# Optimization experiments

Measured on AMD Instinct MI355X. Metric: run time of the kernel, lower is better.

Reference implementation:

```python
import jax, jax.numpy as jnp
import numpy as np

N_NEURONS = 100000
N_EDGES = 5000000
N_TYPES = 64
N_DM = 512
BATCH = 16
LAYER_NUMBER = 4  # number of connectome hops


def setup_inputs() -> dict:
    key = jax.random.key(0)
    ks = jax.random.split(key, 11)
    return {
        "x": jax.random.normal(ks[0], (N_NEURONS, BATCH), dtype=jnp.float32),
        "type_weight": jax.random.normal(ks[1], (N_TYPES,), dtype=jnp.float32),
        "type_bias": jax.random.normal(ks[2], (N_TYPES,), dtype=jnp.float32),
        # shared_weights = log1p(synapse counts) -> positive; use uniform
        "edge_weights": jax.random.uniform(ks[3], (N_EDGES,), dtype=jnp.float32),
        "dm_vals": jax.random.uniform(ks[4], (N_DM,), dtype=jnp.float32),
        "fc_w": jax.random.normal(ks[5], (1, N_DM), dtype=jnp.float32) * 0.04,
        "fc_b": jax.random.normal(ks[6], (1,), dtype=jnp.float32),
        "cell_type_indices": jax.random.randint(ks[7], (N_NEURONS,), 0, N_TYPES),
        "edge_rows": jax.random.randint(ks[8], (N_EDGES,), 0, N_NEURONS),
        "edge_cols": jax.random.randint(ks[9], (N_EDGES,), 0, N_NEURONS),
        "dm_cols": jax.random.randint(ks[10], (N_DM,), 0, N_NEURONS),
    }


def reference(x, type_weight, type_bias, edge_weights, dm_vals, fc_w, fc_b,
              cell_type_indices, edge_rows, edge_cols, dm_cols):
    # RetinaConnectionLayer: per-cell-type 1->1 linear (gathered scale + bias)
    h = x * type_weight[cell_type_indices][:, None] + type_bias[cell_type_indices][:, None]
    # AdultConnectome / SparseMatrixMul: repeated sparse COO matmul h = A @ h
    # with shared per-edge weights, applied layer_number times.
    for _ in range(LAYER_NUMBER):
        contrib = edge_weights[:, None] * h[edge_cols]          # [E, B] gather
        h = jax.ops.segment_sum(contrib, edge_rows, num_segments=N_NEURONS)
    # torch.sparse.mm(decision_making_tensor, h): row-selection sparse matrix
    y = dm_vals[:, None] * h[dm_cols]                           # [N_DM, B]
    # final_fc over the decision-neuron axis
    out = y.T @ fc_w.T + fc_b                                   # [B, 1]
    return out
```

## Files before the change

kernel.cpp:

```cpp
#include <hip/hip_runtime.h>

#define NN 100000
#define NE 5000000
#define NB 16
#define NDM 512

#define RPB 1024
#define NBUCKET 98
#define CAP 55296
#define CHUNK 8192
#define NCHUNK ((NE + CHUNK - 1) / CHUNK)
#define SUB 16
#define NWAVE 16

__global__ void setup(const float* __restrict__ dmv, const int* __restrict__ dmc,
                      const float* __restrict__ fcw,
                      float* __restrict__ u0, int* __restrict__ cursor) {
    int t = threadIdx.x;
    if (t < NDM) atomicAdd(&u0[dmc[t]], dmv[t] * fcw[t]);
    if (t < NBUCKET) cursor[t] = t * CAP;
}

__global__ void scatter_fused(const int* __restrict__ er, const int* __restrict__ ec,
                              const float* __restrict__ ew,
                              const float* __restrict__ u0, float* __restrict__ u1,
                              int* __restrict__ cursor, int2* __restrict__ packed) {
    __shared__ int hist[NWAVE][NBUCKET];
    __shared__ __align__(16) int sdst[CHUNK];
    int tid = threadIdx.x;
    int wv = tid >> 6;
    for (int k = tid; k < NWAVE * NBUCKET; k += 1024) hist[k / NBUCKET][k % NBUCKET] = 0;
    __syncthreads();
    int base = blockIdx.x * CHUNK;
    int n = min(CHUNK, NE - base);
    const int4* ec4 = (const int4*)(ec + base);
    for (int k = tid; k < (n >> 2); k += 1024) {
        int4 c = ec4[k];
        ((int4*)sdst)[k] = c;
        atomicAdd(&hist[wv][c.x >> 10], 1);
        atomicAdd(&hist[wv][c.y >> 10], 1);
        atomicAdd(&hist[wv][c.z >> 10], 1);
        atomicAdd(&hist[wv][c.w >> 10], 1);
    }
    __syncthreads();
    for (int b = tid; b < NBUCKET; b += 1024) {
        int pre[NWAVE];
        int c = 0;
        #pragma unroll
        for (int w = 0; w < NWAVE; ++w) { pre[w] = c; c += hist[w][b]; }
        int gb = c ? atomicAdd(&cursor[b], c) : 0;
        #pragma unroll
        for (int w = 0; w < NWAVE; ++w) hist[w][b] = gb + pre[w];
    }
    __syncthreads();
    const int4*   er4 = (const int4*)(er + base);
    const float4* ew4 = (const float4*)(ew + base);
    for (int k = tid; k < (n >> 2); k += 1024) {
        int4 r = er4[k];
        float4 w = ew4[k];
        int k4 = 4 * k;
        int d, pos;
        float a;
        d = sdst[k4];     pos = atomicAdd(&hist[wv][d >> 10], 1);
        packed[pos] = make_int2(((d & 1023) << 17) | r.x, __float_as_int(w.x));
        a = u0[r.x]; if (a != 0.f) atomicAdd(&u1[d], w.x * a);
        d = sdst[k4 + 1]; pos = atomicAdd(&hist[wv][d >> 10], 1);
        packed[pos] = make_int2(((d & 1023) << 17) | r.y, __float_as_int(w.y));
        a = u0[r.y]; if (a != 0.f) atomicAdd(&u1[d], w.y * a);
        d = sdst[k4 + 2]; pos = atomicAdd(&hist[wv][d >> 10], 1);
        packed[pos] = make_int2(((d & 1023) << 17) | r.z, __float_as_int(w.z));
        a = u0[r.z]; if (a != 0.f) atomicAdd(&u1[d], w.z * a);
        d = sdst[k4 + 3]; pos = atomicAdd(&hist[wv][d >> 10], 1);
        packed[pos] = make_int2(((d & 1023) << 17) | r.w, __float_as_int(w.w));
        a = u0[r.w]; if (a != 0.f) atomicAdd(&u1[d], w.w * a);
    }
}

__global__ void spmv_sorted(const int* __restrict__ cursor,
                            const int2* __restrict__ packed,
                            const float* __restrict__ wc, float* __restrict__ wn) {
    __shared__ float acc[RPB];
    int bucket = blockIdx.x >> 4;
    int sub = blockIdx.x & (SUB - 1);
    int t = threadIdx.x;
    #pragma unroll
    for (int k = 0; k < 4; ++k) acc[t + 256 * k] = 0.f;
    __syncthreads();
    int s = bucket * CAP;
    int e = cursor[bucket];
    int cnt = e - s;
    int slice = (cnt + SUB - 1) >> 4;
    int mys = s + sub * slice;
    int mye = min(mys + slice, e);
    int i = mys + t;
    for (; i + 256 < mye; i += 512) {
        int2 p0 = packed[i];
        int2 p1 = packed[i + 256];
        float v0 = __int_as_float(p0.y) * wc[p0.x & 0x1FFFF];
        float v1 = __int_as_float(p1.y) * wc[p1.x & 0x1FFFF];
        if (v0 != 0.f) atomicAdd(&acc[p0.x >> 17], v0);
        if (v1 != 0.f) atomicAdd(&acc[p1.x >> 17], v1);
    }
    if (i < mye) {
        int2 p = packed[i];
        float v = __int_as_float(p.y) * wc[p.x & 0x1FFFF];
        if (v != 0.f) atomicAdd(&acc[p.x >> 17], v);
    }
    __syncthreads();
    #pragma unroll
    for (int k = 0; k < 4; ++k) {
        int row = bucket * RPB + t + 256 * k;
        float a = acc[t + 256 * k];
        if (a != 0.f && row < NN) atomicAdd(&wn[row], a);
    }
}

__global__ void final_dot(const float* __restrict__ x, const float* __restrict__ tw,
                          const float* __restrict__ tb, const int* __restrict__ ct,
                          const float* __restrict__ u,
                          float* __restrict__ acc_out) {
    __shared__ float s[512];
    __shared__ float sred[256][4];
    __shared__ float sbias[4];
    int tid = threadIdx.x;
    int base = blockIdx.x * 512;
    int nrows = min(512, NN - base);
    float accb = 0.f;
    for (int r = tid; r < nrows; r += 256) {
        int n = base + r;
        float un = u[n];
        int t = ct[n];
        s[r] = un * tw[t];
        accb = fmaf(un, tb[t], accb);
    }
    __syncthreads();
    float a0 = 0.f, a1 = 0.f, a2 = 0.f, a3 = 0.f;
    int j = (tid & 3) * 4;
    for (int r = tid >> 2; r < nrows; r += 64) {
        float4 xv = *(const float4*)&x[(size_t)(base + r) * NB + j];
        float sv = s[r];
        a0 = fmaf(sv, xv.x, a0);
        a1 = fmaf(sv, xv.y, a1);
        a2 = fmaf(sv, xv.z, a2);
        a3 = fmaf(sv, xv.w, a3);
    }
    sred[tid][0] = a0; sred[tid][1] = a1; sred[tid][2] = a2; sred[tid][3] = a3;
    for (int off = 32; off; off >>= 1) accb += __shfl_down(accb, off);
    if ((tid & 63) == 0) sbias[tid >> 6] = accb;
    __syncthreads();
    if (tid < 16) {
        int q = tid >> 2, k = tid & 3;
        float sum = 0.f;
        for (int i = 0; i < 64; ++i) sum += sred[q + 4 * i][k];
        atomicAdd(&acc_out[tid], sum);
    }
    if (tid == 16)
        atomicAdd(&acc_out[16], sbias[0] + sbias[1] + sbias[2] + sbias[3]);
}

__global__ void finalize(const float* __restrict__ acc, const float* __restrict__ fcb,
                         float* __restrict__ out) {
    int b = threadIdx.x;
    if (b < NB) out[b] = acc[b] + acc[16] + fcb[0];
}

extern "C" void kernel_launch(void* const* d_in, const int* in_sizes, int n_in,
                              void* d_out, int out_size, void* d_ws, size_t ws_size,
                              hipStream_t stream) {
    const float* x   = (const float*)d_in[0];
    const float* tw  = (const float*)d_in[1];
    const float* tb  = (const float*)d_in[2];
    const float* ew  = (const float*)d_in[3];
    const float* dmv = (const float*)d_in[4];
    const float* fcw = (const float*)d_in[5];
    const float* fcb = (const float*)d_in[6];
    const int* ct  = (const int*)d_in[7];
    const int* er  = (const int*)d_in[8];
    const int* ec  = (const int*)d_in[9];
    const int* dmc = (const int*)d_in[10];
    float* out = (float*)d_out;

    char* ws = (char*)d_ws;
    float* u   = (float*)ws;
    float* acc = u + 5 * (size_t)NN;
    size_t zero_bytes = (5 * (size_t)NN + 32) * 4;
    ws += zero_bytes;
    int* cursor = (int*)ws;         ws += 128 * 4;
    ws = (char*)(((uintptr_t)ws + 15) & ~(uintptr_t)15);
    int2* packed = (int2*)ws;

    hipMemsetAsync(u, 0, zero_bytes, stream);

    setup<<<1, 512, 0, stream>>>(dmv, dmc, fcw, u, cursor);

    scatter_fused<<<NCHUNK, 1024, 0, stream>>>(er, ec, ew, u, u + NN, cursor, packed);

    for (int l = 1; l < 4; ++l) {
        spmv_sorted<<<NBUCKET * SUB, 256, 0, stream>>>(cursor, packed,
                                                       u + (size_t)l * NN,
                                                       u + (size_t)(l + 1) * NN);
    }

    final_dot<<<(NN + 511) / 512, 256, 0, stream>>>(x, tw, tb, ct, u + 4 * (size_t)NN, acc);
    finalize<<<1, 64, 0, stream>>>(acc, fcb, out);
}
```

Baseline: 170.9 us.

## Stage bucketed edges in shared memory before coalesced global write

The scatter kernel now sorts each chunk's packed edges into bucket order in LDS, using a local exclusive scan of bucket counts, instead of writing each edge straight to its scattered global position. A final pass then copies the LDS buffer to global memory, so consecutive threads write mostly contiguous addresses within each bucket run. This targets the uncoalesced random 8-byte global stores. In exchange it adds about 75KB more LDS per block (lower occupancy), a serial single-thread prefix scan and two extra barriers.

```diff
diff --git a/kernel.cpp b/kernel.cpp
--- a/kernel.cpp
+++ b/kernel.cpp
@@ -27,6 +27,11 @@
                               int* __restrict__ cursor, int2* __restrict__ packed) {
     __shared__ int hist[NWAVE][NBUCKET];
     __shared__ __align__(16) int sdst[CHUNK];
+    __shared__ int2 pval[CHUNK];
+    __shared__ unsigned char sbk[CHUNK];
+    __shared__ int lbloc[NBUCKET];
+    __shared__ int gbase[NBUCKET];
+    __shared__ int ctot[NBUCKET];
     int tid = threadIdx.x;
     int wv = tid >> 6;
     for (int k = tid; k < NWAVE * NBUCKET; k += 1024) hist[k / NBUCKET][k % NBUCKET] = 0;
@@ -43,14 +48,27 @@
         atomicAdd(&hist[wv][c.w >> 10], 1);
     }
     __syncthreads();
-    for (int b = tid; b < NBUCKET; b += 1024) {
-        int pre[NWAVE];
+    int pre[NWAVE];
+    int myb = -1, myc = 0;
+    if (tid < NBUCKET) {
+        myb = tid;
         int c = 0;
         #pragma unroll
-        for (int w = 0; w < NWAVE; ++w) { pre[w] = c; c += hist[w][b]; }
-        int gb = c ? atomicAdd(&cursor[b], c) : 0;
+        for (int w = 0; w < NWAVE; ++w) { pre[w] = c; c += hist[w][myb]; }
+        myc = c;
+        ctot[myb] = c;
+        gbase[myb] = c ? atomicAdd(&cursor[myb], c) : 0;
+    }
+    __syncthreads();
+    if (tid == 0) {
+        int run = 0;
+        for (int b = 0; b < NBUCKET; ++b) { lbloc[b] = run; run += ctot[b]; }
+    }
+    __syncthreads();
+    if (myb >= 0) {
+        int lb = lbloc[myb];
         #pragma unroll
-        for (int w = 0; w < NWAVE; ++w) hist[w][b] = gb + pre[w];
+        for (int w = 0; w < NWAVE; ++w) hist[w][myb] = lb + pre[w];
     }
     __syncthreads();
     const int4*   er4 = (const int4*)(er + base);
@@ -59,20 +77,29 @@
         int4 r = er4[k];
         float4 w = ew4[k];
         int k4 = 4 * k;
-        int d, pos;
+        int d, bk, lp;
         float a;
-        d = sdst[k4];     pos = atomicAdd(&hist[wv][d >> 10], 1);
-        packed[pos] = make_int2(((d & 1023) << 17) | r.x, __float_as_int(w.x));
+        d = sdst[k4];     bk = d >> 10; lp = atomicAdd(&hist[wv][bk], 1);
+        pval[lp] = make_int2(((d & 1023) << 17) | r.x, __float_as_int(w.x));
+        sbk[lp] = (unsigned char)bk;
         a = u0[r.x]; if (a != 0.f) atomicAdd(&u1[d], w.x * a);
-        d = sdst[k4 + 1]; pos = atomicAdd(&hist[wv][d >> 10], 1);
-        packed[pos] = make_int2(((d & 1023) << 17) | r.y, __float_as_int(w.y));
+        d = sdst[k4 + 1]; bk = d >> 10; lp = atomicAdd(&hist[wv][bk], 1);
+        pval[lp] = make_int2(((d & 1023) << 17) | r.y, __float_as_int(w.y));
+        sbk[lp] = (unsigned char)bk;
         a = u0[r.y]; if (a != 0.f) atomicAdd(&u1[d], w.y * a);
-        d = sdst[k4 + 2]; pos = atomicAdd(&hist[wv][d >> 10], 1);
-        packed[pos] = make_int2(((d & 1023) << 17) | r.z, __float_as_int(w.z));
+        d = sdst[k4 + 2]; bk = d >> 10; lp = atomicAdd(&hist[wv][bk], 1);
+        pval[lp] = make_int2(((d & 1023) << 17) | r.z, __float_as_int(w.z));
+        sbk[lp] = (unsigned char)bk;
         a = u0[r.z]; if (a != 0.f) atomicAdd(&u1[d], w.z * a);
-        d = sdst[k4 + 3]; pos = atomicAdd(&hist[wv][d >> 10], 1);
-        packed[pos] = make_int2(((d & 1023) << 17) | r.w, __float_as_int(w.w));
+        d = sdst[k4 + 3]; bk = d >> 10; lp = atomicAdd(&hist[wv][bk], 1);
+        pval[lp] = make_int2(((d & 1023) << 17) | r.w, __float_as_int(w.w));
+        sbk[lp] = (unsigned char)bk;
         a = u0[r.w]; if (a != 0.f) atomicAdd(&u1[d], w.w * a);
+    }
+    __syncthreads();
+    for (int i = tid; i < n; i += 1024) {
+        int bk = sbk[i];
+        packed[gbase[bk] + (i - lbloc[bk])] = pval[i];
     }
 }
 
```

Result: faster. 158.5 us (-7.2%).
